# Kernel optimization log

Hardware: AMD Instinct MI355X
Metric: run time of the kernel (lower is better)

The kernel has to match this reference:

```python
import jax, jax.numpy as jnp
import numpy as np

N_PP = 8192      # number of papers (nodes_num_pp)
N_A = 8192       # number of authors
N_AP = N_PP + N_A  # nodes_num_ap (stacked paper+author id space)
DIM = 16
E = 262144
ALPHA = 0.5


def _cdist(x, y):
    # Euclidean cdist via Gram trick; avoids (B, A, D) broadcast intermediate.
    x2 = jnp.sum(x * x, axis=-1)[:, None]
    y2 = jnp.sum(y * y, axis=-1)[None, :]
    d2 = x2 + y2 - 2.0 * (x @ y.T)
    return jnp.sqrt(jnp.maximum(d2, 0.0))


def setup_inputs() -> dict:
    key = jax.random.key(0)
    ks = jax.random.split(key, 8)
    p_star = jax.random.normal(ks[0], (N_PP, DIM), dtype=jnp.float32)
    p = jax.random.normal(ks[1], (N_PP, DIM), dtype=jnp.float32)
    a = jax.random.normal(ks[2], (N_A, DIM), dtype=jnp.float32)
    beta_ap = 2.0 * jax.random.uniform(ks[3], (N_AP,), dtype=jnp.float32) - 1.0
    gamma_pp = 2.0 * jax.random.uniform(ks[4], (2 * N_PP,), dtype=jnp.float32) - 1.0
    edges_pp = jax.random.randint(ks[5], (2, E), 0, N_PP)
    e_ap0 = jax.random.randint(ks[6], (E,), 0, N_PP)
    e_ap1 = jax.random.randint(ks[7], (E,), N_PP, N_AP)
    edges_ap = jnp.stack([e_ap0, e_ap1])
    p_star_nodes = jnp.arange(N_PP, dtype=jnp.int32)
    p_nodes = jnp.arange(N_PP, dtype=jnp.int32)
    a_nodes = jnp.arange(N_A, dtype=jnp.int32) + N_PP
    return {"p_star": p_star, "p": p, "a": a, "beta_ap": beta_ap,
            "gamma_pp": gamma_pp, "edges_pp": edges_pp, "edges_ap": edges_ap,
            "p_star_nodes": p_star_nodes, "p_nodes": p_nodes, "a_nodes": a_nodes}


def reference(p_star, p, a, beta_ap, gamma_pp, edges_pp, edges_ap,
              p_star_nodes, p_nodes, a_nodes):
    # ---------- paper-paper (pp) term ----------
    ps_sel = p_star[p_star_nodes]                    # (B, D)
    p_sel = p[p_nodes]                               # (P, D)
    g_ps = gamma_pp[p_star_nodes]                    # (B,)
    g_p = gamma_pp[p_nodes + N_PP]                   # (P,)
    # gamma_mat.T - dist_mat, shape (B, P)
    m_pp = jnp.exp(g_ps[:, None] + g_p[None, :] - _cdist(ps_sel, p_sel))
    nonlink_pp = jnp.sum(jnp.triu(m_pp, k=1))        # strict upper triangle
    gamma_pair = gamma_pp[edges_pp[0]] + gamma_pp[edges_pp[1] + N_PP]
    d_pp = jnp.linalg.norm(p_star[edges_pp[0]] - p[edges_pp[1]], axis=-1)
    link_pp = jnp.sum(gamma_pair - d_pp)
    nll_pp = -(link_pp - nonlink_pp)

    # ---------- author-paper (ap) term ----------
    a_sel = a[a_nodes - N_PP]                        # (A, D)
    b_ps = beta_ap[p_star_nodes]                     # (B,)
    b_a = beta_ap[a_nodes]                           # (A,)
    # intended math: beta_mat.T - dist_mat, shape (B, A)
    m_ap = jnp.exp(b_ps[:, None] + b_a[None, :] - _cdist(ps_sel, a_sel))
    nonlink_ap = jnp.sum(m_ap)
    beta_pair = beta_ap[edges_ap[0]] + beta_ap[edges_ap[1]]
    d_ap = jnp.linalg.norm(p_star[edges_ap[0]] - a[edges_ap[1] - N_PP], axis=-1)
    link_ap = jnp.sum(beta_pair - d_ap)
    nll_ap = -(link_ap - nonlink_ap)

    n_p = p_nodes.shape[0]
    n_a = a_nodes.shape[0]
    return ALPHA * nll_pp / n_p + (1.0 - ALPHA) * nll_ap / n_a
```

## Files before the change

### kernel.cpp

```cpp
#include <hip/hip_runtime.h>
#include <stdint.h>

#define N_PP   8192
#define DIM    16
#define NEDGE  262144
#define LOG2E  1.4426950408889634f

#define WS_EDGE  8
#define WS_PSBF  512
#define WS_PBF   (WS_PSBF + 65536)
#define WS_ABF   (WS_PBF  + 65536)
#define WS_X2PS  (WS_ABF  + 65536)
#define WS_Y2P   (WS_X2PS + 8192)
#define WS_Y2A   (WS_Y2P  + 8192)
#define WS_EGC   (WS_Y2A  + 8192)
#define WS_EBC   (WS_EGC  + 8192)
#define WS_GL2   (WS_EBC  + 8192)
#define WS_BL2   (WS_GL2  + 8192)

#define NQ_AP  1024
#define NQ_PP  544
#define NB_MAT (NQ_AP + NQ_PP)

typedef short    bf16x8 __attribute__((ext_vector_type(8)));
typedef float    f32x4  __attribute__((ext_vector_type(4)));
typedef unsigned u32x4  __attribute__((ext_vector_type(4)));

__device__ __forceinline__ float waveReduce(float v) {
#pragma unroll
    for (int off = 32; off > 0; off >>= 1)
        v += __shfl_down(v, off, 64);
    return v;
}

__device__ __forceinline__ unsigned bf16_rne(float f) {
    unsigned u = __builtin_bit_cast(unsigned, f);
    return (u + 0x7FFFu + ((u >> 16) & 1u)) >> 16;
}
__device__ __forceinline__ unsigned packbf2(float a, float b) {
    return bf16_rne(a) | (bf16_rne(b) << 16);
}

__device__ __forceinline__ void gload_lds(const uint32_t* g, uint32_t* l) {
    __builtin_amdgcn_global_load_lds(
        (const __attribute__((address_space(1))) void*)(uintptr_t)g,
        (__attribute__((address_space(3))) void*)(unsigned)(uintptr_t)l,
        16, 0, 0);
}

__global__ __launch_bounds__(256) void pre_kernel(
    const float* __restrict__ p_star, const float* __restrict__ p,
    const float* __restrict__ a, const float* __restrict__ beta_ap,
    const float* __restrict__ gamma_pp, const int* __restrict__ edges_pp,
    const int* __restrict__ edges_ap, float* __restrict__ ws)
{
    const int b = blockIdx.x, tid = threadIdx.x;

    if (b < 224) {
        const int g = b * 256 + tid;
        if (g < 8) ws[g] = 0.0f;
        if (g < 3 * 8192) {
            const int arr = g >> 13, idx = g & 8191;
            const float* src = arr == 0 ? p_star : (arr == 1 ? p : a);
            const int bfo = arr == 0 ? WS_PSBF : (arr == 1 ? WS_PBF : WS_ABF);
            const int n2o = arr == 0 ? WS_X2PS : (arr == 1 ? WS_Y2P : WS_Y2A);
            const float4* rp = (const float4*)(src + idx * DIM);
            float4 f0 = rp[0], f1 = rp[1], f2 = rp[2], f3 = rp[3];
            float n2 = f0.x*f0.x + f0.y*f0.y + f0.z*f0.z + f0.w*f0.w
                     + f1.x*f1.x + f1.y*f1.y + f1.z*f1.z + f1.w*f1.w
                     + f2.x*f2.x + f2.y*f2.y + f2.z*f2.z + f2.w*f2.w
                     + f3.x*f3.x + f3.y*f3.y + f3.z*f3.z + f3.w*f3.w;
            u32x4 u0 = { packbf2(f0.x, f0.y), packbf2(f0.z, f0.w),
                         packbf2(f1.x, f1.y), packbf2(f1.z, f1.w) };
            u32x4 u1 = { packbf2(f2.x, f2.y), packbf2(f2.z, f2.w),
                         packbf2(f3.x, f3.y), packbf2(f3.z, f3.w) };
            u32x4* dst = (u32x4*)(ws + bfo) + idx * 2;
            dst[0] = u0; dst[1] = u1;
            ws[n2o + idx] = n2;
        } else if (g < 7 * 8192) {
            const int h = g - 3 * 8192, q = h >> 13, i = h & 8191;
            if      (q == 0) ws[WS_EGC + i] = __expf(gamma_pp[8192 + i]);
            else if (q == 1) ws[WS_EBC + i] = __expf(beta_ap[8192 + i]);
            else if (q == 2) ws[WS_GL2 + i] = gamma_pp[i] * LOG2E;
            else             ws[WS_BL2 + i] = beta_ap[i] * LOG2E;
        }
    } else {
        __shared__ float smred[4];
        const int  eb   = b - 224;
        const bool isPP = (eb < 128);
        const int  base = (isPP ? eb : eb - 128) * 2048;
        float sum = 0.f;
#pragma unroll
        for (int k = 0; k < 8; ++k) {
            const int e = base + k * 256 + tid;
            const float* yrow;
            float bias;
            int e0;
            if (isPP) {
                e0 = edges_pp[e];
                int e1 = edges_pp[NEDGE + e];
                yrow = p + e1 * DIM;
                bias = gamma_pp[e0] + gamma_pp[N_PP + e1];
            } else {
                e0 = edges_ap[e];
                int e1 = edges_ap[NEDGE + e];
                yrow = a + (e1 - N_PP) * DIM;
                bias = beta_ap[e0] + beta_ap[e1];
            }
            const float4* xp = (const float4*)(p_star + e0 * DIM);
            const float4* yp = (const float4*)yrow;
            float d2 = 0.f;
#pragma unroll
            for (int kk = 0; kk < 4; ++kk) {
                float4 xv = xp[kk], yv = yp[kk];
                float dx = xv.x - yv.x, dy = xv.y - yv.y,
                      dz = xv.z - yv.z, dw = xv.w - yv.w;
                d2 += dx*dx + dy*dy + dz*dz + dw*dw;
            }
            sum += bias - __builtin_amdgcn_sqrtf(d2);
        }
        float wsum = waveReduce(sum);
        if ((tid & 63) == 0) smred[tid >> 6] = wsum;
        __syncthreads();
        if (tid == 0)
            ws[WS_EDGE + eb] = smred[0] + smred[1] + smred[2] + smred[3];
    }
}

__global__ void main_kernel(float* __restrict__ ws, float* __restrict__ out)
{
    __shared__ uint32_t sbuf[5120];
    __shared__ float smred[4];
    const int b = blockIdx.x, tid = threadIdx.x, wid = tid >> 6;
    const int lane = tid & 63, quad = lane >> 4, l16 = lane & 15;

    const bool isPP = (b >= NQ_AP);
    int g, c;
    if (!isPP) { g = b >> 4; c = b & 15; }
    else {
        const int qq = b - NQ_AP;
        int bnd = 0;
        while (2 * (bnd + 1) * (bnd + 2) <= qq) ++bnd;
        const int r = qq - 2 * bnd * (bnd + 1);
        g = 4 * bnd + r / (bnd + 1);
        c = r % (bnd + 1);
    }
    const int t0 = c << 5;

    const uint32_t* Xbf = (const uint32_t*)(ws + WS_PSBF);
    const uint32_t* Ybf = (const uint32_t*)(ws + (isPP ? WS_PBF : WS_ABF));
    const float* x2a = ws + WS_X2PS;
    const float* y2  = ws + (isPP ? WS_Y2P : WS_Y2A);
    const float* gl2 = ws + (isPP ? WS_GL2 : WS_BL2);
    const float* EcA = ws + (isPP ? WS_EGC : WS_EBC);

    const int sA = (g << 3) + (wid << 1);
    bf16x8 bfrag[2];
    float  y2c[2], Ec[2];
#pragma unroll
    for (int ss = 0; ss < 2; ++ss) {
        const int j = ((sA + ss) << 4) + l16;
        u32x4 bu = {0u, 0u, 0u, 0u};
        if (quad < 2) bu = *(const u32x4*)(Ybf + j * 8 + (quad << 2));
        bfrag[ss] = __builtin_bit_cast(bf16x8, bu);
        y2c[ss] = y2[j];
        Ec[ss]  = EcA[j];
    }

    for (int k = wid; k < 20; k += 4) {
        const uint32_t* gsrc;
        int loff;
        if (k < 16)      { gsrc = Xbf + (t0 << 7) + (k << 8);            loff = k << 8; }
        else if (k < 18) { gsrc = (const uint32_t*)(x2a + (t0 << 4)) + ((k - 16) << 8);
                           loff = 4096 + ((k - 16) << 8); }
        else             { gsrc = (const uint32_t*)(gl2 + (t0 << 4)) + ((k - 18) << 8);
                           loff = 4608 + ((k - 18) << 8); }
        gload_lds(gsrc + (lane << 2), &sbuf[loff]);
    }
    __syncthreads();

    const f32x4 zero4 = {0.f, 0.f, 0.f, 0.f};
    float acc[2] = {0.f, 0.f};
    const int tHi = isPP ? (sA + 1 < t0 + 32 ? sA + 2 : t0 + 32) : t0 + 32;
    for (int t = t0; t < tHi; ++t) {
        const int tl = t - t0;
        const u32x4 au = *(const u32x4*)&sbuf[(tl << 7) + (l16 << 3) + ((quad & 1) << 2)];
        const f32x4 x24 = *(const f32x4*)((const float*)sbuf + 4096 + (tl << 4) + (quad << 2));
        const f32x4 ag4 = *(const f32x4*)((const float*)sbuf + 4608 + (tl << 4) + (quad << 2));
#pragma unroll
        for (int ss = 0; ss < 2; ++ss) {
            const int s = sA + ss;
            if (isPP && t > s) continue;
            f32x4 d = __builtin_amdgcn_mfma_f32_16x16x32_bf16(
                __builtin_bit_cast(bf16x8, au), bfrag[ss], zero4, 0, 0, 0);
            if (!isPP || t < s) {
#pragma unroll
                for (int r = 0; r < 4; ++r) {
                    float d2 = fmaf(-2.f, d[r], x24[r] + y2c[ss]);
                    d2 = fmaxf(d2, 0.f);
                    acc[ss] += __builtin_amdgcn_exp2f(
                        fmaf(-LOG2E, __builtin_amdgcn_sqrtf(d2), ag4[r]));
                }
            } else {
#pragma unroll
                for (int r = 0; r < 4; ++r) {
                    float d2 = fmaf(-2.f, d[r], x24[r] + y2c[ss]);
                    d2 = fmaxf(d2, 0.f);
                    float term = __builtin_amdgcn_exp2f(
                        fmaf(-LOG2E, __builtin_amdgcn_sqrtf(d2), ag4[r]));
                    if (l16 <= (quad << 2) + r) term = 0.f;
                    acc[ss] += term;
                }
            }
        }
    }
    const float val = acc[0] * Ec[0] + acc[1] * Ec[1];

    float wsum = waveReduce(val);
    if ((tid & 63) == 0) smred[wid] = wsum;
    __syncthreads();
    if (tid == 0) {
        atomicAdd(&ws[isPP ? 2 : 0], smred[0] + smred[1] + smred[2] + smred[3]);
        __threadfence();
        unsigned old = atomicAdd((unsigned*)(ws + 4), 1u);
        if (old == NB_MAT - 1) {
            float s0 = atomicAdd(&ws[0], 0.f);
            float s2 = atomicAdd(&ws[2], 0.f);
            float lpp = 0.f, lap = 0.f;
            for (int i = 0; i < 128; i += 4) {
                const float4 v = *(const float4*)(ws + WS_EDGE + i);
                const float4 u = *(const float4*)(ws + WS_EDGE + 128 + i);
                lpp += v.x + v.y + v.z + v.w;
                lap += u.x + u.y + u.z + u.w;
            }
            out[0] = 0.5f * (s0 - lpp) / (float)N_PP
                   + 0.5f * (s2 - lap) / (float)N_PP;
        }
    }
}

extern "C" void kernel_launch(void* const* d_in, const int* in_sizes, int n_in,
                              void* d_out, int out_size, void* d_ws, size_t ws_size,
                              hipStream_t stream) {
    const float* p_star   = (const float*)d_in[0];
    const float* p        = (const float*)d_in[1];
    const float* a        = (const float*)d_in[2];
    const float* beta_ap  = (const float*)d_in[3];
    const float* gamma_pp = (const float*)d_in[4];
    const int*   edges_pp = (const int*)d_in[5];
    const int*   edges_ap = (const int*)d_in[6];

    float* ws  = (float*)d_ws;
    float* out = (float*)d_out;

    hipLaunchKernelGGL(pre_kernel, dim3(480), dim3(256), 0, stream,
                       p_star, p, a, beta_ap, gamma_pp, edges_pp, edges_ap, ws);
    hipLaunchKernelGGL(main_kernel, dim3(NB_MAT), dim3(256), 0, stream, ws, out);
}
```

Baseline: 138.7 us.

## Fuse preprocessing, edge sums and pairwise tiles into one kernel with 32x32 MFMA

Merges the preprocessing kernel into the main kernel. Each tile block now converts its 512 p_star rows to bf16 and computes norms and biases directly into LDS, and each wave builds its own B fragment from the raw inputs. The 16x16x32 MFMA is replaced by a 32x32x16 MFMA, so each wave handles one 32-column strip over 16 row subtiles with the next A fragment prefetched. Edge-sum blocks join the same grid and accumulate with atomics, and a memset clears the counters. This removes one launch and the workspace round trip, but repeats the per-tile bf16 conversion and changes per-wave work granularity.

```diff
diff --git a/kernel.cpp b/kernel.cpp
--- a/kernel.cpp
+++ b/kernel.cpp
@@ -6,24 +6,15 @@
 #define NEDGE  262144
 #define LOG2E  1.4426950408889634f
 
-#define WS_EDGE  8
-#define WS_PSBF  512
-#define WS_PBF   (WS_PSBF + 65536)
-#define WS_ABF   (WS_PBF  + 65536)
-#define WS_X2PS  (WS_ABF  + 65536)
-#define WS_Y2P   (WS_X2PS + 8192)
-#define WS_Y2A   (WS_Y2P  + 8192)
-#define WS_EGC   (WS_Y2A  + 8192)
-#define WS_EBC   (WS_EGC  + 8192)
-#define WS_GL2   (WS_EBC  + 8192)
-#define WS_BL2   (WS_GL2  + 8192)
-
-#define NQ_AP  1024
-#define NQ_PP  544
-#define NB_MAT (NQ_AP + NQ_PP)
+#define NB_EDGE 256
+#define NQ_AP   1024
+#define NQ_PP   544
+#define NB_TOT  (NB_EDGE + NQ_AP + NQ_PP)
+
 
 typedef short    bf16x8 __attribute__((ext_vector_type(8)));
 typedef float    f32x4  __attribute__((ext_vector_type(4)));
+typedef float    f32x16 __attribute__((ext_vector_type(16)));
 typedef unsigned u32x4  __attribute__((ext_vector_type(4)));
 
 __device__ __forceinline__ float waveReduce(float v) {
@@ -41,200 +32,189 @@
     return bf16_rne(a) | (bf16_rne(b) << 16);
 }
 
-__device__ __forceinline__ void gload_lds(const uint32_t* g, uint32_t* l) {
-    __builtin_amdgcn_global_load_lds(
-        (const __attribute__((address_space(1))) void*)(uintptr_t)g,
-        (__attribute__((address_space(3))) void*)(unsigned)(uintptr_t)l,
-        16, 0, 0);
-}
-
-__global__ __launch_bounds__(256) void pre_kernel(
+__global__ __launch_bounds__(256) void fused_kernel(
     const float* __restrict__ p_star, const float* __restrict__ p,
     const float* __restrict__ a, const float* __restrict__ beta_ap,
     const float* __restrict__ gamma_pp, const int* __restrict__ edges_pp,
-    const int* __restrict__ edges_ap, float* __restrict__ ws)
+    const int* __restrict__ edges_ap, float* __restrict__ ws,
+    float* __restrict__ out)
 {
+    __shared__ uint32_t sbuf[5120];
+    __shared__ float smred[4];
     const int b = blockIdx.x, tid = threadIdx.x;
-
-    if (b < 224) {
-        const int g = b * 256 + tid;
-        if (g < 8) ws[g] = 0.0f;
-        if (g < 3 * 8192) {
-            const int arr = g >> 13, idx = g & 8191;
-            const float* src = arr == 0 ? p_star : (arr == 1 ? p : a);
-            const int bfo = arr == 0 ? WS_PSBF : (arr == 1 ? WS_PBF : WS_ABF);
-            const int n2o = arr == 0 ? WS_X2PS : (arr == 1 ? WS_Y2P : WS_Y2A);
-            const float4* rp = (const float4*)(src + idx * DIM);
-            float4 f0 = rp[0], f1 = rp[1], f2 = rp[2], f3 = rp[3];
-            float n2 = f0.x*f0.x + f0.y*f0.y + f0.z*f0.z + f0.w*f0.w
-                     + f1.x*f1.x + f1.y*f1.y + f1.z*f1.z + f1.w*f1.w
-                     + f2.x*f2.x + f2.y*f2.y + f2.z*f2.z + f2.w*f2.w
-                     + f3.x*f3.x + f3.y*f3.y + f3.z*f3.z + f3.w*f3.w;
-            u32x4 u0 = { packbf2(f0.x, f0.y), packbf2(f0.z, f0.w),
-                         packbf2(f1.x, f1.y), packbf2(f1.z, f1.w) };
-            u32x4 u1 = { packbf2(f2.x, f2.y), packbf2(f2.z, f2.w),
-                         packbf2(f3.x, f3.y), packbf2(f3.z, f3.w) };
-            u32x4* dst = (u32x4*)(ws + bfo) + idx * 2;
-            dst[0] = u0; dst[1] = u1;
-            ws[n2o + idx] = n2;
-        } else if (g < 7 * 8192) {
-            const int h = g - 3 * 8192, q = h >> 13, i = h & 8191;
-            if      (q == 0) ws[WS_EGC + i] = __expf(gamma_pp[8192 + i]);
-            else if (q == 1) ws[WS_EBC + i] = __expf(beta_ap[8192 + i]);
-            else if (q == 2) ws[WS_GL2 + i] = gamma_pp[i] * LOG2E;
-            else             ws[WS_BL2 + i] = beta_ap[i] * LOG2E;
-        }
-    } else {
-        __shared__ float smred[4];
-        const int  eb   = b - 224;
-        const bool isPP = (eb < 128);
-        const int  base = (isPP ? eb : eb - 128) * 2048;
+    const int wid = tid >> 6, lane = tid & 63;
+
+    if (b < NB_EDGE) {
+        const bool isPPe = (b < 128);
+        const int  base  = (isPPe ? b : b - 128) * 2048;
         float sum = 0.f;
 #pragma unroll
         for (int k = 0; k < 8; ++k) {
             const int e = base + k * 256 + tid;
-            const float* yrow;
-            float bias;
-            int e0;
-            if (isPP) {
+            const float* yrow; float bias; int e0;
+            if (isPPe) {
                 e0 = edges_pp[e];
-                int e1 = edges_pp[NEDGE + e];
+                const int e1 = edges_pp[NEDGE + e];
                 yrow = p + e1 * DIM;
                 bias = gamma_pp[e0] + gamma_pp[N_PP + e1];
             } else {
                 e0 = edges_ap[e];
-                int e1 = edges_ap[NEDGE + e];
+                const int e1 = edges_ap[NEDGE + e];
                 yrow = a + (e1 - N_PP) * DIM;
                 bias = beta_ap[e0] + beta_ap[e1];
             }
-            const float4* xp = (const float4*)(p_star + e0 * DIM);
-            const float4* yp = (const float4*)yrow;
+            const float4* xp4 = (const float4*)(p_star + e0 * DIM);
+            const float4* yp4 = (const float4*)yrow;
             float d2 = 0.f;
 #pragma unroll
             for (int kk = 0; kk < 4; ++kk) {
-                float4 xv = xp[kk], yv = yp[kk];
-                float dx = xv.x - yv.x, dy = xv.y - yv.y,
-                      dz = xv.z - yv.z, dw = xv.w - yv.w;
+                const float4 xv = xp4[kk], yv = yp4[kk];
+                const float dx = xv.x - yv.x, dy = xv.y - yv.y,
+                            dz = xv.z - yv.z, dw = xv.w - yv.w;
                 d2 += dx*dx + dy*dy + dz*dz + dw*dw;
             }
             sum += bias - __builtin_amdgcn_sqrtf(d2);
         }
-        float wsum = waveReduce(sum);
-        if ((tid & 63) == 0) smred[tid >> 6] = wsum;
+        const float wsum = waveReduce(sum);
+        if ((tid & 63) == 0) smred[wid] = wsum;
         __syncthreads();
         if (tid == 0)
-            ws[WS_EDGE + eb] = smred[0] + smred[1] + smred[2] + smred[3];
-    }
-}
-
-__global__ void main_kernel(float* __restrict__ ws, float* __restrict__ out)
-{
-    __shared__ uint32_t sbuf[5120];
-    __shared__ float smred[4];
-    const int b = blockIdx.x, tid = threadIdx.x, wid = tid >> 6;
-    const int lane = tid & 63, quad = lane >> 4, l16 = lane & 15;
-
-    const bool isPP = (b >= NQ_AP);
-    int g, c;
-    if (!isPP) { g = b >> 4; c = b & 15; }
-    else {
-        const int qq = b - NQ_AP;
-        int bnd = 0;
-        while (2 * (bnd + 1) * (bnd + 2) <= qq) ++bnd;
-        const int r = qq - 2 * bnd * (bnd + 1);
-        g = 4 * bnd + r / (bnd + 1);
-        c = r % (bnd + 1);
-    }
-    const int t0 = c << 5;
-
-    const uint32_t* Xbf = (const uint32_t*)(ws + WS_PSBF);
-    const uint32_t* Ybf = (const uint32_t*)(ws + (isPP ? WS_PBF : WS_ABF));
-    const float* x2a = ws + WS_X2PS;
-    const float* y2  = ws + (isPP ? WS_Y2P : WS_Y2A);
-    const float* gl2 = ws + (isPP ? WS_GL2 : WS_BL2);
-    const float* EcA = ws + (isPP ? WS_EGC : WS_EBC);
-
-    const int sA = (g << 3) + (wid << 1);
-    bf16x8 bfrag[2];
-    float  y2c[2], Ec[2];
-#pragma unroll
-    for (int ss = 0; ss < 2; ++ss) {
-        const int j = ((sA + ss) << 4) + l16;
-        u32x4 bu = {0u, 0u, 0u, 0u};
-        if (quad < 2) bu = *(const u32x4*)(Ybf + j * 8 + (quad << 2));
-        bfrag[ss] = __builtin_bit_cast(bf16x8, bu);
-        y2c[ss] = y2[j];
-        Ec[ss]  = EcA[j];
-    }
-
-    for (int k = wid; k < 20; k += 4) {
-        const uint32_t* gsrc;
-        int loff;
-        if (k < 16)      { gsrc = Xbf + (t0 << 7) + (k << 8);            loff = k << 8; }
-        else if (k < 18) { gsrc = (const uint32_t*)(x2a + (t0 << 4)) + ((k - 16) << 8);
-                           loff = 4096 + ((k - 16) << 8); }
-        else             { gsrc = (const uint32_t*)(gl2 + (t0 << 4)) + ((k - 18) << 8);
-                           loff = 4608 + ((k - 18) << 8); }
-        gload_lds(gsrc + (lane << 2), &sbuf[loff]);
-    }
-    __syncthreads();
-
-    const f32x4 zero4 = {0.f, 0.f, 0.f, 0.f};
-    float acc[2] = {0.f, 0.f};
-    const int tHi = isPP ? (sA + 1 < t0 + 32 ? sA + 2 : t0 + 32) : t0 + 32;
-    for (int t = t0; t < tHi; ++t) {
-        const int tl = t - t0;
-        const u32x4 au = *(const u32x4*)&sbuf[(tl << 7) + (l16 << 3) + ((quad & 1) << 2)];
-        const f32x4 x24 = *(const f32x4*)((const float*)sbuf + 4096 + (tl << 4) + (quad << 2));
-        const f32x4 ag4 = *(const f32x4*)((const float*)sbuf + 4608 + (tl << 4) + (quad << 2));
-#pragma unroll
-        for (int ss = 0; ss < 2; ++ss) {
-            const int s = sA + ss;
-            if (isPP && t > s) continue;
-            f32x4 d = __builtin_amdgcn_mfma_f32_16x16x32_bf16(
-                __builtin_bit_cast(bf16x8, au), bfrag[ss], zero4, 0, 0, 0);
-            if (!isPP || t < s) {
-#pragma unroll
-                for (int r = 0; r < 4; ++r) {
-                    float d2 = fmaf(-2.f, d[r], x24[r] + y2c[ss]);
+            atomicAdd(&ws[isPPe ? 1 : 3],
+                      smred[0] + smred[1] + smred[2] + smred[3]);
+    } else {
+        const int  b2   = b - NB_EDGE;
+        const bool isPP = (b2 >= NQ_AP);
+        int g, c;
+        if (!isPP) { g = b2 >> 4; c = b2 & 15; }
+        else {
+            const int qq = b2 - NQ_AP;
+            int bnd = 0;
+            while (2 * (bnd + 1) * (bnd + 2) <= qq) ++bnd;
+            const int r = qq - 2 * bnd * (bnd + 1);
+            g = 4 * bnd + r / (bnd + 1);
+            c = r % (bnd + 1);
+        }
+        const int R0 = c << 9;
+        const int lane31 = lane & 31, kh = lane >> 5;
+
+        const float* Ysrc = isPP ? p : a;
+        const float* rB   = isPP ? gamma_pp : beta_ap;
+        const float* cBi  = (isPP ? gamma_pp : beta_ap) + N_PP;
+
+        for (int rr = tid; rr < 512; rr += 256) {
+            const float4* rp = (const float4*)(p_star + (R0 + rr) * DIM);
+            const float4 f0 = rp[0], f1 = rp[1], f2 = rp[2], f3 = rp[3];
+            const float n2 =
+                f0.x*f0.x + f0.y*f0.y + f0.z*f0.z + f0.w*f0.w +
+                f1.x*f1.x + f1.y*f1.y + f1.z*f1.z + f1.w*f1.w +
+                f2.x*f2.x + f2.y*f2.y + f2.z*f2.z + f2.w*f2.w +
+                f3.x*f3.x + f3.y*f3.y + f3.z*f3.z + f3.w*f3.w;
+            const u32x4 u0 = { packbf2(f0.x,f0.y), packbf2(f0.z,f0.w),
+                               packbf2(f1.x,f1.y), packbf2(f1.z,f1.w) };
+            const u32x4 u1 = { packbf2(f2.x,f2.y), packbf2(f2.z,f2.w),
+                               packbf2(f3.x,f3.y), packbf2(f3.z,f3.w) };
+            *(u32x4*)&sbuf[rr * 8]     = u0;
+            *(u32x4*)&sbuf[rr * 8 + 4] = u1;
+            float2 xb;
+            xb.x = n2;
+            xb.y = rB[R0 + rr] * LOG2E;
+            *(float2*)((float*)sbuf + 4096 + rr * 2) = xb;
+        }
+
+        const int s = (g << 2) + wid;
+        const int j = (s << 5) + lane31;
+        const float4* yp4 = (const float4*)(Ysrc + j * DIM);
+        const float4 yv0 = yp4[0], yv1 = yp4[1], yv2 = yp4[2], yv3 = yp4[3];
+        const float y2c =
+            yv0.x*yv0.x + yv0.y*yv0.y + yv0.z*yv0.z + yv0.w*yv0.w +
+            yv1.x*yv1.x + yv1.y*yv1.y + yv1.z*yv1.z + yv1.w*yv1.w +
+            yv2.x*yv2.x + yv2.y*yv2.y + yv2.z*yv2.z + yv2.w*yv2.w +
+            yv3.x*yv3.x + yv3.y*yv3.y + yv3.z*yv3.z + yv3.w*yv3.w;
+        const float4 ha = kh ? yv2 : yv0, hb = kh ? yv3 : yv1;
+        const u32x4 bupk = { packbf2(ha.x,ha.y), packbf2(ha.z,ha.w),
+                             packbf2(hb.x,hb.y), packbf2(hb.z,hb.w) };
+        const bf16x8 bfrag = __builtin_bit_cast(bf16x8, bupk);
+        const float Ec = __expf(cBi[j]);
+
+        __syncthreads();
+
+        const int sl    = s - (c << 4);
+        const int tlEnd = isPP ? (sl < 15 ? sl : 15) : 15;
+        const int dTl   = isPP ? sl : -1;
+        const int aoff  = (lane31 << 3) + (kh << 2);
+        const float* xbb = (const float*)sbuf + 4096 + (kh << 3);
+        const int kh4 = kh << 2;
+
+        const f32x16 zero16 = {0.f,0.f,0.f,0.f,0.f,0.f,0.f,0.f,
+                               0.f,0.f,0.f,0.f,0.f,0.f,0.f,0.f};
+        float acc0 = 0.f, acc1 = 0.f, acc2 = 0.f, acc3 = 0.f;
+
+        u32x4 a_cur = *(const u32x4*)&sbuf[aoff];
+        for (int tl = 0; tl <= tlEnd; ++tl) {
+            const f32x16 dm = __builtin_amdgcn_mfma_f32_32x32x16_bf16(
+                __builtin_bit_cast(bf16x8, a_cur), bfrag, zero16, 0, 0, 0);
+            if (tl < tlEnd)
+                a_cur = *(const u32x4*)&sbuf[((tl + 1) << 8) + aoff];
+            const float* xb = xbb + (tl << 6);
+            f32x4 xp[8];
+            xp[0] = *(const f32x4*)(xb +  0);
+            xp[1] = *(const f32x4*)(xb +  4);
+            xp[2] = *(const f32x4*)(xb + 16);
+            xp[3] = *(const f32x4*)(xb + 20);
+            xp[4] = *(const f32x4*)(xb + 32);
+            xp[5] = *(const f32x4*)(xb + 36);
+            xp[6] = *(const f32x4*)(xb + 48);
+            xp[7] = *(const f32x4*)(xb + 52);
+            if (tl != dTl) {
+#pragma unroll
+                for (int q = 0; q < 16; ++q) {
+                    float d2 = fmaf(-2.f, dm[q],
+                                    xp[q >> 1][(q & 1) << 1] + y2c);
                     d2 = fmaxf(d2, 0.f);
-                    acc[ss] += __builtin_amdgcn_exp2f(
-                        fmaf(-LOG2E, __builtin_amdgcn_sqrtf(d2), ag4[r]));
+                    const float t = __builtin_amdgcn_exp2f(
+                        fmaf(-LOG2E, __builtin_amdgcn_sqrtf(d2),
+                             xp[q >> 1][((q & 1) << 1) + 1]));
+                    if ((q & 3) == 0) acc0 += t;
+                    else if ((q & 3) == 1) acc1 += t;
+                    else if ((q & 3) == 2) acc2 += t;
+                    else acc3 += t;
                 }
             } else {
 #pragma unroll
-                for (int r = 0; r < 4; ++r) {
-                    float d2 = fmaf(-2.f, d[r], x24[r] + y2c[ss]);
+                for (int q = 0; q < 16; ++q) {
+                    float d2 = fmaf(-2.f, dm[q],
+                                    xp[q >> 1][(q & 1) << 1] + y2c);
                     d2 = fmaxf(d2, 0.f);
-                    float term = __builtin_amdgcn_exp2f(
-                        fmaf(-LOG2E, __builtin_amdgcn_sqrtf(d2), ag4[r]));
-                    if (l16 <= (quad << 2) + r) term = 0.f;
-                    acc[ss] += term;
+                    float t = __builtin_amdgcn_exp2f(
+                        fmaf(-LOG2E, __builtin_amdgcn_sqrtf(d2),
+                             xp[q >> 1][((q & 1) << 1) + 1]));
+                    const int rq = (q & 3) + ((q >> 2) << 3) + kh4;
+                    if (lane31 <= rq) t = 0.f;
+                    if ((q & 3) == 0) acc0 += t;
+                    else if ((q & 3) == 1) acc1 += t;
+                    else if ((q & 3) == 2) acc2 += t;
+                    else acc3 += t;
                 }
             }
         }
+        const float val = (acc0 + acc1 + acc2 + acc3) * Ec;
+        const float wsum = waveReduce(val);
+        if ((tid & 63) == 0) smred[wid] = wsum;
+        __syncthreads();
+        if (tid == 0)
+            atomicAdd(&ws[isPP ? 0 : 2],
+                      smred[0] + smred[1] + smred[2] + smred[3]);
     }
-    const float val = acc[0] * Ec[0] + acc[1] * Ec[1];
-
-    float wsum = waveReduce(val);
-    if ((tid & 63) == 0) smred[wid] = wsum;
-    __syncthreads();
+
+    __threadfence();
     if (tid == 0) {
-        atomicAdd(&ws[isPP ? 2 : 0], smred[0] + smred[1] + smred[2] + smred[3]);
-        __threadfence();
-        unsigned old = atomicAdd((unsigned*)(ws + 4), 1u);
-        if (old == NB_MAT - 1) {
-            float s0 = atomicAdd(&ws[0], 0.f);
-            float s2 = atomicAdd(&ws[2], 0.f);
-            float lpp = 0.f, lap = 0.f;
-            for (int i = 0; i < 128; i += 4) {
-                const float4 v = *(const float4*)(ws + WS_EDGE + i);
-                const float4 u = *(const float4*)(ws + WS_EDGE + 128 + i);
-                lpp += v.x + v.y + v.z + v.w;
-                lap += u.x + u.y + u.z + u.w;
-            }
-            out[0] = 0.5f * (s0 - lpp) / (float)N_PP
-                   + 0.5f * (s2 - lap) / (float)N_PP;
+        const unsigned old = atomicAdd((unsigned*)(ws + 4), 1u);
+        if (old == NB_TOT - 1) {
+            const float s0 = atomicAdd(&ws[0], 0.f);
+            const float l1 = atomicAdd(&ws[1], 0.f);
+            const float s2 = atomicAdd(&ws[2], 0.f);
+            const float l3 = atomicAdd(&ws[3], 0.f);
+            out[0] = 0.5f * ((s0 - l1) + (s2 - l3)) / (float)N_PP;
         }
     }
 }
@@ -250,10 +230,8 @@
     const int*   edges_pp = (const int*)d_in[5];
     const int*   edges_ap = (const int*)d_in[6];
 
-    float* ws  = (float*)d_ws;
-    float* out = (float*)d_out;
-
-    hipLaunchKernelGGL(pre_kernel, dim3(480), dim3(256), 0, stream,
-                       p_star, p, a, beta_ap, gamma_pp, edges_pp, edges_ap, ws);
-    hipLaunchKernelGGL(main_kernel, dim3(NB_MAT), dim3(256), 0, stream, ws, out);
-}
+    hipMemsetAsync(d_ws, 0, 32, stream);
+    hipLaunchKernelGGL(fused_kernel, dim3(NB_TOT), dim3(256), 0, stream,
+                       p_star, p, a, beta_ap, gamma_pp, edges_pp, edges_ap,
+                       (float*)d_ws, (float*)d_out);
+}
```

New measurement: 233.1 us. 1.68x slower.

## Move edge-sum blocks into main kernel and halve pairwise tile size

Applied to the files above, without the earlier changes.

Moves the 256 edge-gather blocks from the preprocessing kernel into the main kernel, so gather-heavy edge work can overlap with the MFMA pairwise blocks. Each pairwise block now covers 16 rows instead of 32, which doubles the block count and halves shared memory use, aiming at better load balance and occupancy. Edge sums are now accumulated with atomics instead of per-block slots, and the zeroing of the accumulators moves to a hipMemsetAsync. The extra memset launch and the larger number of blocks add overhead.

```diff
diff --git a/kernel.cpp b/kernel.cpp
--- a/kernel.cpp
+++ b/kernel.cpp
@@ -6,7 +6,6 @@
 #define NEDGE  262144
 #define LOG2E  1.4426950408889634f
 
-#define WS_EDGE  8
 #define WS_PSBF  512
 #define WS_PBF   (WS_PSBF + 65536)
 #define WS_ABF   (WS_PBF  + 65536)
@@ -18,9 +17,10 @@
 #define WS_GL2   (WS_EBC  + 8192)
 #define WS_BL2   (WS_GL2  + 8192)
 
-#define NQ_AP  1024
-#define NQ_PP  544
-#define NB_MAT (NQ_AP + NQ_PP)
+#define NB_EDGE 256
+#define NQ_AP   2048
+#define NQ_PP   1056
+#define NB_TOT  (NB_EDGE + NQ_AP + NQ_PP)
 
 typedef short    bf16x8 __attribute__((ext_vector_type(8)));
 typedef float    f32x4  __attribute__((ext_vector_type(4)));
@@ -51,190 +51,186 @@
 __global__ __launch_bounds__(256) void pre_kernel(
     const float* __restrict__ p_star, const float* __restrict__ p,
     const float* __restrict__ a, const float* __restrict__ beta_ap,
+    const float* __restrict__ gamma_pp, float* __restrict__ ws)
+{
+    const int g = blockIdx.x * 256 + threadIdx.x;
+    if (g < 3 * 8192) {
+        const int arr = g >> 13, idx = g & 8191;
+        const float* src = arr == 0 ? p_star : (arr == 1 ? p : a);
+        const int bfo = arr == 0 ? WS_PSBF : (arr == 1 ? WS_PBF : WS_ABF);
+        const int n2o = arr == 0 ? WS_X2PS : (arr == 1 ? WS_Y2P : WS_Y2A);
+        const float4* rp = (const float4*)(src + idx * DIM);
+        float4 f0 = rp[0], f1 = rp[1], f2 = rp[2], f3 = rp[3];
+        float n2 = f0.x*f0.x + f0.y*f0.y + f0.z*f0.z + f0.w*f0.w
+                 + f1.x*f1.x + f1.y*f1.y + f1.z*f1.z + f1.w*f1.w
+                 + f2.x*f2.x + f2.y*f2.y + f2.z*f2.z + f2.w*f2.w
+                 + f3.x*f3.x + f3.y*f3.y + f3.z*f3.z + f3.w*f3.w;
+        u32x4 u0 = { packbf2(f0.x, f0.y), packbf2(f0.z, f0.w),
+                     packbf2(f1.x, f1.y), packbf2(f1.z, f1.w) };
+        u32x4 u1 = { packbf2(f2.x, f2.y), packbf2(f2.z, f2.w),
+                     packbf2(f3.x, f3.y), packbf2(f3.z, f3.w) };
+        u32x4* dst = (u32x4*)(ws + bfo) + idx * 2;
+        dst[0] = u0; dst[1] = u1;
+        ws[n2o + idx] = n2;
+    } else {
+        const int h = g - 3 * 8192, q = h >> 13, i = h & 8191;
+        if      (q == 0) ws[WS_EGC + i] = __expf(gamma_pp[8192 + i]);
+        else if (q == 1) ws[WS_EBC + i] = __expf(beta_ap[8192 + i]);
+        else if (q == 2) ws[WS_GL2 + i] = gamma_pp[i] * LOG2E;
+        else             ws[WS_BL2 + i] = beta_ap[i] * LOG2E;
+    }
+}
+
+__global__ __launch_bounds__(256) void main_kernel(
+    const float* __restrict__ p_star, const float* __restrict__ p,
+    const float* __restrict__ a, const float* __restrict__ beta_ap,
     const float* __restrict__ gamma_pp, const int* __restrict__ edges_pp,
-    const int* __restrict__ edges_ap, float* __restrict__ ws)
+    const int* __restrict__ edges_ap, float* __restrict__ ws,
+    float* __restrict__ out)
 {
+    __shared__ uint32_t sbuf[2560];
+    __shared__ float smred[4];
     const int b = blockIdx.x, tid = threadIdx.x;
-
-    if (b < 224) {
-        const int g = b * 256 + tid;
-        if (g < 8) ws[g] = 0.0f;
-        if (g < 3 * 8192) {
-            const int arr = g >> 13, idx = g & 8191;
-            const float* src = arr == 0 ? p_star : (arr == 1 ? p : a);
-            const int bfo = arr == 0 ? WS_PSBF : (arr == 1 ? WS_PBF : WS_ABF);
-            const int n2o = arr == 0 ? WS_X2PS : (arr == 1 ? WS_Y2P : WS_Y2A);
-            const float4* rp = (const float4*)(src + idx * DIM);
-            float4 f0 = rp[0], f1 = rp[1], f2 = rp[2], f3 = rp[3];
-            float n2 = f0.x*f0.x + f0.y*f0.y + f0.z*f0.z + f0.w*f0.w
-                     + f1.x*f1.x + f1.y*f1.y + f1.z*f1.z + f1.w*f1.w
-                     + f2.x*f2.x + f2.y*f2.y + f2.z*f2.z + f2.w*f2.w
-                     + f3.x*f3.x + f3.y*f3.y + f3.z*f3.z + f3.w*f3.w;
-            u32x4 u0 = { packbf2(f0.x, f0.y), packbf2(f0.z, f0.w),
-                         packbf2(f1.x, f1.y), packbf2(f1.z, f1.w) };
-            u32x4 u1 = { packbf2(f2.x, f2.y), packbf2(f2.z, f2.w),
-                         packbf2(f3.x, f3.y), packbf2(f3.z, f3.w) };
-            u32x4* dst = (u32x4*)(ws + bfo) + idx * 2;
-            dst[0] = u0; dst[1] = u1;
-            ws[n2o + idx] = n2;
-        } else if (g < 7 * 8192) {
-            const int h = g - 3 * 8192, q = h >> 13, i = h & 8191;
-            if      (q == 0) ws[WS_EGC + i] = __expf(gamma_pp[8192 + i]);
-            else if (q == 1) ws[WS_EBC + i] = __expf(beta_ap[8192 + i]);
-            else if (q == 2) ws[WS_GL2 + i] = gamma_pp[i] * LOG2E;
-            else             ws[WS_BL2 + i] = beta_ap[i] * LOG2E;
-        }
-    } else {
-        __shared__ float smred[4];
-        const int  eb   = b - 224;
-        const bool isPP = (eb < 128);
-        const int  base = (isPP ? eb : eb - 128) * 2048;
+    const int wid = tid >> 6, lane = tid & 63;
+
+    if (b < NB_EDGE) {
+        const bool isPPe = (b < 128);
+        const int  base  = (isPPe ? b : b - 128) * 2048;
         float sum = 0.f;
 #pragma unroll
         for (int k = 0; k < 8; ++k) {
             const int e = base + k * 256 + tid;
-            const float* yrow;
-            float bias;
-            int e0;
-            if (isPP) {
+            const float* yrow; float bias; int e0;
+            if (isPPe) {
                 e0 = edges_pp[e];
-                int e1 = edges_pp[NEDGE + e];
+                const int e1 = edges_pp[NEDGE + e];
                 yrow = p + e1 * DIM;
                 bias = gamma_pp[e0] + gamma_pp[N_PP + e1];
             } else {
                 e0 = edges_ap[e];
-                int e1 = edges_ap[NEDGE + e];
+                const int e1 = edges_ap[NEDGE + e];
                 yrow = a + (e1 - N_PP) * DIM;
                 bias = beta_ap[e0] + beta_ap[e1];
             }
-            const float4* xp = (const float4*)(p_star + e0 * DIM);
-            const float4* yp = (const float4*)yrow;
+            const float4* xp4 = (const float4*)(p_star + e0 * DIM);
+            const float4* yp4 = (const float4*)yrow;
             float d2 = 0.f;
 #pragma unroll
             for (int kk = 0; kk < 4; ++kk) {
-                float4 xv = xp[kk], yv = yp[kk];
-                float dx = xv.x - yv.x, dy = xv.y - yv.y,
-                      dz = xv.z - yv.z, dw = xv.w - yv.w;
+                const float4 xv = xp4[kk], yv = yp4[kk];
+                const float dx = xv.x - yv.x, dy = xv.y - yv.y,
+                            dz = xv.z - yv.z, dw = xv.w - yv.w;
                 d2 += dx*dx + dy*dy + dz*dz + dw*dw;
             }
             sum += bias - __builtin_amdgcn_sqrtf(d2);
         }
-        float wsum = waveReduce(sum);
-        if ((tid & 63) == 0) smred[tid >> 6] = wsum;
+        const float wsum = waveReduce(sum);
+        if ((tid & 63) == 0) smred[wid] = wsum;
         __syncthreads();
         if (tid == 0)
-            ws[WS_EDGE + eb] = smred[0] + smred[1] + smred[2] + smred[3];
-    }
-}
-
-__global__ void main_kernel(float* __restrict__ ws, float* __restrict__ out)
-{
-    __shared__ uint32_t sbuf[5120];
-    __shared__ float smred[4];
-    const int b = blockIdx.x, tid = threadIdx.x, wid = tid >> 6;
-    const int lane = tid & 63, quad = lane >> 4, l16 = lane & 15;
-
-    const bool isPP = (b >= NQ_AP);
-    int g, c;
-    if (!isPP) { g = b >> 4; c = b & 15; }
-    else {
-        const int qq = b - NQ_AP;
-        int bnd = 0;
-        while (2 * (bnd + 1) * (bnd + 2) <= qq) ++bnd;
-        const int r = qq - 2 * bnd * (bnd + 1);
-        g = 4 * bnd + r / (bnd + 1);
-        c = r % (bnd + 1);
-    }
-    const int t0 = c << 5;
-
-    const uint32_t* Xbf = (const uint32_t*)(ws + WS_PSBF);
-    const uint32_t* Ybf = (const uint32_t*)(ws + (isPP ? WS_PBF : WS_ABF));
-    const float* x2a = ws + WS_X2PS;
-    const float* y2  = ws + (isPP ? WS_Y2P : WS_Y2A);
-    const float* gl2 = ws + (isPP ? WS_GL2 : WS_BL2);
-    const float* EcA = ws + (isPP ? WS_EGC : WS_EBC);
-
-    const int sA = (g << 3) + (wid << 1);
-    bf16x8 bfrag[2];
-    float  y2c[2], Ec[2];
-#pragma unroll
-    for (int ss = 0; ss < 2; ++ss) {
-        const int j = ((sA + ss) << 4) + l16;
-        u32x4 bu = {0u, 0u, 0u, 0u};
-        if (quad < 2) bu = *(const u32x4*)(Ybf + j * 8 + (quad << 2));
-        bfrag[ss] = __builtin_bit_cast(bf16x8, bu);
-        y2c[ss] = y2[j];
-        Ec[ss]  = EcA[j];
-    }
-
-    for (int k = wid; k < 20; k += 4) {
-        const uint32_t* gsrc;
-        int loff;
-        if (k < 16)      { gsrc = Xbf + (t0 << 7) + (k << 8);            loff = k << 8; }
-        else if (k < 18) { gsrc = (const uint32_t*)(x2a + (t0 << 4)) + ((k - 16) << 8);
-                           loff = 4096 + ((k - 16) << 8); }
-        else             { gsrc = (const uint32_t*)(gl2 + (t0 << 4)) + ((k - 18) << 8);
-                           loff = 4608 + ((k - 18) << 8); }
-        gload_lds(gsrc + (lane << 2), &sbuf[loff]);
-    }
-    __syncthreads();
-
-    const f32x4 zero4 = {0.f, 0.f, 0.f, 0.f};
-    float acc[2] = {0.f, 0.f};
-    const int tHi = isPP ? (sA + 1 < t0 + 32 ? sA + 2 : t0 + 32) : t0 + 32;
-    for (int t = t0; t < tHi; ++t) {
-        const int tl = t - t0;
-        const u32x4 au = *(const u32x4*)&sbuf[(tl << 7) + (l16 << 3) + ((quad & 1) << 2)];
-        const f32x4 x24 = *(const f32x4*)((const float*)sbuf + 4096 + (tl << 4) + (quad << 2));
-        const f32x4 ag4 = *(const f32x4*)((const float*)sbuf + 4608 + (tl << 4) + (quad << 2));
+            atomicAdd(&ws[isPPe ? 1 : 3],
+                      smred[0] + smred[1] + smred[2] + smred[3]);
+    } else {
+        const int  b2   = b - NB_EDGE;
+        const bool isPP = (b2 >= NQ_AP);
+        int g, c;
+        if (!isPP) { g = b2 >> 5; c = b2 & 31; }
+        else {
+            const int qq = b2 - NQ_AP;
+            int m = 0;
+            while ((m + 1) * (m + 2) <= qq) ++m;
+            const int r = qq - m * (m + 1);
+            g = 2 * m + r / (m + 1);
+            c = r % (m + 1);
+        }
+        const int t0 = c << 4;
+        const int quad = lane >> 4, l16 = lane & 15;
+
+        const uint32_t* Xbf = (const uint32_t*)(ws + WS_PSBF);
+        const uint32_t* Ybf = (const uint32_t*)(ws + (isPP ? WS_PBF : WS_ABF));
+        const float* x2a = ws + WS_X2PS;
+        const float* y2  = ws + (isPP ? WS_Y2P : WS_Y2A);
+        const float* gl2 = ws + (isPP ? WS_GL2 : WS_BL2);
+        const float* EcA = ws + (isPP ? WS_EGC : WS_EBC);
+
+        const int sA = (g << 3) + (wid << 1);
+        bf16x8 bfrag[2];
+        float  y2c[2], Ec[2];
 #pragma unroll
         for (int ss = 0; ss < 2; ++ss) {
-            const int s = sA + ss;
-            if (isPP && t > s) continue;
-            f32x4 d = __builtin_amdgcn_mfma_f32_16x16x32_bf16(
-                __builtin_bit_cast(bf16x8, au), bfrag[ss], zero4, 0, 0, 0);
-            if (!isPP || t < s) {
-#pragma unroll
-                for (int r = 0; r < 4; ++r) {
-                    float d2 = fmaf(-2.f, d[r], x24[r] + y2c[ss]);
-                    d2 = fmaxf(d2, 0.f);
-                    acc[ss] += __builtin_amdgcn_exp2f(
-                        fmaf(-LOG2E, __builtin_amdgcn_sqrtf(d2), ag4[r]));
-                }
-            } else {
-#pragma unroll
-                for (int r = 0; r < 4; ++r) {
-                    float d2 = fmaf(-2.f, d[r], x24[r] + y2c[ss]);
-                    d2 = fmaxf(d2, 0.f);
-                    float term = __builtin_amdgcn_exp2f(
-                        fmaf(-LOG2E, __builtin_amdgcn_sqrtf(d2), ag4[r]));
-                    if (l16 <= (quad << 2) + r) term = 0.f;
-                    acc[ss] += term;
+            const int j = ((sA + ss) << 4) + l16;
+            u32x4 bu = {0u, 0u, 0u, 0u};
+            if (quad < 2) bu = *(const u32x4*)(Ybf + j * 8 + (quad << 2));
+            bfrag[ss] = __builtin_bit_cast(bf16x8, bu);
+            y2c[ss] = y2[j];
+            Ec[ss]  = EcA[j];
+        }
+
+        for (int k = wid; k < 10; k += 4) {
+            const uint32_t* gsrc;
+            int loff;
+            if (k < 8)       { gsrc = Xbf + (c << 11) + (k << 8); loff = k << 8; }
+            else if (k == 8) { gsrc = (const uint32_t*)(x2a + (c << 8)); loff = 2048; }
+            else             { gsrc = (const uint32_t*)(gl2 + (c << 8)); loff = 2304; }
+            gload_lds(gsrc + (lane << 2), &sbuf[loff]);
+        }
+        __syncthreads();
+
+        const f32x4 zero4 = {0.f, 0.f, 0.f, 0.f};
+        float acc[2] = {0.f, 0.f};
+        const int tEnd = t0 + 16;
+        const int tHi  = isPP ? (sA + 2 < tEnd ? sA + 2 : tEnd) : tEnd;
+        for (int t = t0; t < tHi; ++t) {
+            const int tl = t - t0;
+            const u32x4 au = *(const u32x4*)&sbuf[(tl << 7) + (l16 << 3) + ((quad & 1) << 2)];
+            const f32x4 x24 = *(const f32x4*)((const float*)sbuf + 2048 + (tl << 4) + (quad << 2));
+            const f32x4 ag4 = *(const f32x4*)((const float*)sbuf + 2304 + (tl << 4) + (quad << 2));
+#pragma unroll
+            for (int ss = 0; ss < 2; ++ss) {
+                const int s = sA + ss;
+                if (isPP && t > s) continue;
+                f32x4 d = __builtin_amdgcn_mfma_f32_16x16x32_bf16(
+                    __builtin_bit_cast(bf16x8, au), bfrag[ss], zero4, 0, 0, 0);
+                if (!isPP || t < s) {
+#pragma unroll
+                    for (int r = 0; r < 4; ++r) {
+                        float d2 = fmaf(-2.f, d[r], x24[r] + y2c[ss]);
+                        d2 = fmaxf(d2, 0.f);
+                        acc[ss] += __builtin_amdgcn_exp2f(
+                            fmaf(-LOG2E, __builtin_amdgcn_sqrtf(d2), ag4[r]));
+                    }
+                } else {
+#pragma unroll
+                    for (int r = 0; r < 4; ++r) {
+                        float d2 = fmaf(-2.f, d[r], x24[r] + y2c[ss]);
+                        d2 = fmaxf(d2, 0.f);
+                        float term = __builtin_amdgcn_exp2f(
+                            fmaf(-LOG2E, __builtin_amdgcn_sqrtf(d2), ag4[r]));
+                        if (l16 <= (quad << 2) + r) term = 0.f;
+                        acc[ss] += term;
+                    }
                 }
             }
         }
+        const float val = acc[0] * Ec[0] + acc[1] * Ec[1];
+
+        const float wsum = waveReduce(val);
+        if ((tid & 63) == 0) smred[wid] = wsum;
+        __syncthreads();
+        if (tid == 0)
+            atomicAdd(&ws[isPP ? 0 : 2],
+                      smred[0] + smred[1] + smred[2] + smred[3]);
     }
-    const float val = acc[0] * Ec[0] + acc[1] * Ec[1];
-
-    float wsum = waveReduce(val);
-    if ((tid & 63) == 0) smred[wid] = wsum;
-    __syncthreads();
+
+    __threadfence();
     if (tid == 0) {
-        atomicAdd(&ws[isPP ? 2 : 0], smred[0] + smred[1] + smred[2] + smred[3]);
-        __threadfence();
-        unsigned old = atomicAdd((unsigned*)(ws + 4), 1u);
-        if (old == NB_MAT - 1) {
-            float s0 = atomicAdd(&ws[0], 0.f);
-            float s2 = atomicAdd(&ws[2], 0.f);
-            float lpp = 0.f, lap = 0.f;
-            for (int i = 0; i < 128; i += 4) {
-                const float4 v = *(const float4*)(ws + WS_EDGE + i);
-                const float4 u = *(const float4*)(ws + WS_EDGE + 128 + i);
-                lpp += v.x + v.y + v.z + v.w;
-                lap += u.x + u.y + u.z + u.w;
-            }
-            out[0] = 0.5f * (s0 - lpp) / (float)N_PP
-                   + 0.5f * (s2 - lap) / (float)N_PP;
+        const unsigned old = atomicAdd((unsigned*)(ws + 4), 1u);
+        if (old == NB_TOT - 1) {
+            const float s0 = atomicAdd(&ws[0], 0.f);
+            const float l1 = atomicAdd(&ws[1], 0.f);
+            const float s2 = atomicAdd(&ws[2], 0.f);
+            const float l3 = atomicAdd(&ws[3], 0.f);
+            out[0] = 0.5f * ((s0 - l1) + (s2 - l3)) / (float)N_PP;
         }
     }
 }
@@ -253,7 +249,10 @@
     float* ws  = (float*)d_ws;
     float* out = (float*)d_out;
 
-    hipLaunchKernelGGL(pre_kernel, dim3(480), dim3(256), 0, stream,
-                       p_star, p, a, beta_ap, gamma_pp, edges_pp, edges_ap, ws);
-    hipLaunchKernelGGL(main_kernel, dim3(NB_MAT), dim3(256), 0, stream, ws, out);
-}
+    hipMemsetAsync(d_ws, 0, 32, stream);
+    hipLaunchKernelGGL(pre_kernel, dim3(224), dim3(256), 0, stream,
+                       p_star, p, a, beta_ap, gamma_pp, ws);
+    hipLaunchKernelGGL(main_kernel, dim3(NB_TOT), dim3(256), 0, stream,
+                       p_star, p, a, beta_ap, gamma_pp, edges_pp, edges_ap,
+                       ws, out);
+}
```

Result: slower. 303.3 us (+118.8%).
